# Kernel optimization log

Hardware: AMD Instinct MI355X
Metric: run time of the kernel (lower is better)

Reference implementation:

```python
import jax, jax.numpy as jnp
import numpy as np

B, S, D = 8, 1024, 1024
H = 16
D_HEAD = D // H
RANK = 256
NC = 64
NE = 64
KC = 16  # top_k_compress
KE = 8   # top_k_expand


def setup_inputs() -> dict:
    key = jax.random.key(0)
    ks = jax.random.split(key, 9)
    rn = lambda k, sh, s=1.0: jax.random.normal(k, sh, jnp.float32) * s
    return {
        "x": rn(ks[0], (B, S, D)),
        "importance": jax.random.uniform(ks[1], (B, S), jnp.float32),
        "W_compress": rn(ks[2], (NC, D), 1.0 / np.sqrt(D)),
        "W_Q": rn(ks[3], (NE, D), 1.0 / np.sqrt(D)),
        "W_K": rn(ks[4], (NE, D), 1.0 / np.sqrt(D)),
        "W_V": rn(ks[5], (NE, D), 1.0 / np.sqrt(D)),
        "compress_neurons": rn(ks[6], (NC, D, RANK), 1.0 / np.sqrt(D)),
        "expand_pool": rn(ks[7], (NE, RANK, D), 1.0 / np.sqrt(RANK)),
        "W_O": rn(ks[8], (D, D), 1.0 / np.sqrt(D)),
    }


def _route(x, importance, W, k):
    """Per-token softmax router, importance-aggregated, top-k renormalized."""
    pref = jax.nn.softmax(jnp.einsum('bsd,nd->bsn', x, W), axis=-1)  # [B,S,n]
    w = jnp.einsum('bs,bsn->bn', importance, pref)                   # [B,n]
    w = w / (w.sum(-1, keepdims=True) + 1e-8)
    tw, ti = jax.lax.top_k(w, k)                                     # [B,k]
    tw = tw / (tw.sum(-1, keepdims=True) + 1e-8)
    return tw, ti


def reference(x, importance, W_compress, W_Q, W_K, W_V, compress_neurons, expand_pool, W_O):
    # --- GlobalRouters.get_attention_weights ---
    cw, ci = _route(x, importance, W_compress, KC)
    qw, qi = _route(x, importance, W_Q, KE)
    kw, ki = _route(x, importance, W_K, KE)
    vw, vi = _route(x, importance, W_V, KE)

    # --- NeuronCircuit.forward ---
    # gather + mix compress neurons: [B,KC,D,R] -> [B,D,R]
    shared_c = jnp.einsum('bk,bkdr->bdr', cw, compress_neurons[ci])
    h = jnp.einsum('bsd,bdr->bsr', x, shared_c)  # [B,S,R]

    eQ = jnp.einsum('bk,bkrd->brd', qw, expand_pool[qi])
    eK = jnp.einsum('bk,bkrd->brd', kw, expand_pool[ki])
    eV = jnp.einsum('bk,bkrd->brd', vw, expand_pool[vi])

    def heads(t):  # [B,S,D] -> [B,H,S,d_head]
        return t.reshape(B, S, H, D_HEAD).transpose(0, 2, 1, 3)

    Q = heads(jnp.einsum('bsr,brd->bsd', h, eQ))
    K = heads(jnp.einsum('bsr,brd->bsd', h, eK))
    V = heads(jnp.einsum('bsr,brd->bsd', h, eV))

    scale = 1.0 / np.sqrt(D_HEAD)
    scores = jnp.einsum('bhqd,bhkd->bhqk', Q, K) * scale
    causal = jnp.tril(jnp.ones((S, S), dtype=bool))
    scores = jnp.where(causal, scores, jnp.finfo(scores.dtype).min)
    attn = jax.nn.softmax(scores, axis=-1)
    out = jnp.einsum('bhqk,bhkd->bhqd', attn, V)
    out = out.transpose(0, 2, 1, 3).reshape(B, S, D)
    return jnp.einsum('bsd,ed->bse', out, W_O)  # expand_O (Linear, no bias)
```

## Files before the change

kernel.cpp:

```cpp
#include <hip/hip_runtime.h>

typedef __attribute__((ext_vector_type(8))) short short8;
typedef __attribute__((ext_vector_type(4))) short short4v;
typedef __attribute__((ext_vector_type(4))) float f32x4;
typedef unsigned short u16;
typedef unsigned int u32;

__device__ __forceinline__ float bf2f(u16 h) {
    return __uint_as_float(((u32)h) << 16);
}
__device__ __forceinline__ u16 f2bf(float f) {
    u32 u = __float_as_uint(f);
    u32 r = u + 0x7fffu + ((u >> 16) & 1u);
    return (u16)(r >> 16);
}
__device__ __forceinline__ u32 pack_bf(float a, float b) {
    return __builtin_amdgcn_perm(__float_as_uint(b), __float_as_uint(a), 0x07060302u);
}

__device__ __forceinline__ void async_copy16(const void* g, void* l) {
    __builtin_amdgcn_global_load_lds(
        (const __attribute__((address_space(1))) void*)g,
        (__attribute__((address_space(3))) void*)l, 16, 0, 0);
}

__global__ __launch_bounds__(256) void cvt_split(
    const float* __restrict__ in, u16* __restrict__ hi, u16* __restrict__ lo, int n4)
{
    int i = blockIdx.x * 256 + threadIdx.x;
    if (i >= n4) return;
    float4 v = ((const float4*)in)[i];
    short4v h, l;
    float vv[4] = {v.x, v.y, v.z, v.w};
#pragma unroll
    for (int j = 0; j < 4; j++) {
        u16 hb = f2bf(vv[j]);
        h[j] = (short)hb;
        l[j] = (short)f2bf(vv[j] - bf2f(hb));
    }
    ((short4v*)hi)[i] = h;
    ((short4v*)lo)[i] = l;
}

__global__ __launch_bounds__(256) void cvt_split_w4(
    const float* __restrict__ w0, const float* __restrict__ w1,
    const float* __restrict__ w2, const float* __restrict__ w3,
    u16* __restrict__ hi, u16* __restrict__ lo)
{
    const int r = blockIdx.x >> 6;
    const float* src = (r == 0) ? w0 : (r == 1) ? w1 : (r == 2) ? w2 : w3;
    int i = (blockIdx.x & 63) * 256 + threadIdx.x;
    float4 v = ((const float4*)src)[i];
    short4v h, l;
    float vv[4] = {v.x, v.y, v.z, v.w};
#pragma unroll
    for (int j = 0; j < 4; j++) {
        u16 hb = f2bf(vv[j]);
        h[j] = (short)hb;
        l[j] = (short)f2bf(vv[j] - bf2f(hb));
    }
    ((short4v*)(hi + (long)r * 65536))[i] = h;
    ((short4v*)(lo + (long)r * 65536))[i] = l;
}

__global__ __launch_bounds__(256) void cvt_bf(
    const float* __restrict__ in, u16* __restrict__ out, int n4)
{
    int i = blockIdx.x * 256 + threadIdx.x;
    if (i >= n4) return;
    float4 v = ((const float4*)in)[i];
    short4v h;
    h[0] = (short)f2bf(v.x); h[1] = (short)f2bf(v.y);
    h[2] = (short)f2bf(v.z); h[3] = (short)f2bf(v.w);
    ((short4v*)out)[i] = h;
}

template <typename CT>
__global__ __launch_bounds__(256) void gemm_bt(
    const u16* __restrict__ A, long lda, long bsA,
    const u16* __restrict__ Bm, long ldb, long bsB,
    CT* __restrict__ C, long ldc, long bsC, int K, float cscale)
{
    __shared__ __align__(16) u16 lsA[128 * 64];
    __shared__ __align__(16) u16 lsB[128 * 64];
    const int tid = threadIdx.x;
    const int wave = tid >> 6, lane = tid & 63;
    const int quad = lane >> 4, l15 = lane & 15;
    const int wm = wave >> 1, wn = wave & 1;
    const long m0 = (long)blockIdx.x * 128, n0 = (long)blockIdx.y * 128;
    A  += (long)blockIdx.z * bsA;
    Bm += (long)blockIdx.z * bsB;
    C  += (long)blockIdx.z * bsC;
    const int srow = lane >> 2, scol = (lane & 3) * 8;

    f32x4 acc[4][4];
#pragma unroll
    for (int i = 0; i < 4; i++)
#pragma unroll
        for (int j = 0; j < 4; j++) acc[i][j] = (f32x4){0.f, 0.f, 0.f, 0.f};

    const u16* ga0 = A + (m0 + (wave * 2 + 0) * 16 + srow) * lda + scol;
    const u16* ga1 = A + (m0 + (wave * 2 + 1) * 16 + srow) * lda + scol;
    const u16* gb0 = Bm + (n0 + (wave * 2 + 0) * 16 + srow) * ldb + scol;
    const u16* gb1 = Bm + (n0 + (wave * 2 + 1) * 16 + srow) * ldb + scol;
    u16* laA = &lsA[(wave * 2 + 0) * 1024];
    u16* laB = &lsA[(wave * 2 + 1) * 1024];
    u16* lbA = &lsB[(wave * 2 + 0) * 1024];
    u16* lbB = &lsB[(wave * 2 + 1) * 1024];

    for (int kk = 0; kk < K; kk += 64) {
        async_copy16(ga0 + kk,      laA);
        async_copy16(ga0 + kk + 32, laA + 512);
        async_copy16(ga1 + kk,      laB);
        async_copy16(ga1 + kk + 32, laB + 512);
        async_copy16(gb0 + kk,      lbA);
        async_copy16(gb0 + kk + 32, lbA + 512);
        async_copy16(gb1 + kk,      lbB);
        async_copy16(gb1 + kk + 32, lbB + 512);
        __syncthreads();
#pragma unroll
        for (int kb = 0; kb < 2; kb++) {
            short8 af[4], bf[4];
#pragma unroll
            for (int mt = 0; mt < 4; mt++)
                af[mt] = *(const short8*)&lsA[(wm * 4 + mt) * 1024 + kb * 512 + l15 * 32 + quad * 8];
#pragma unroll
            for (int nt = 0; nt < 4; nt++)
                bf[nt] = *(const short8*)&lsB[(wn * 4 + nt) * 1024 + kb * 512 + l15 * 32 + quad * 8];
#pragma unroll
            for (int mt = 0; mt < 4; mt++)
#pragma unroll
                for (int nt = 0; nt < 4; nt++)
                    acc[mt][nt] = __builtin_amdgcn_mfma_f32_16x16x32_bf16(
                        af[mt], bf[nt], acc[mt][nt], 0, 0, 0);
        }
        __syncthreads();
    }
#pragma unroll
    for (int mt = 0; mt < 4; mt++) {
        const long rowb = m0 + wm * 64 + mt * 16 + quad * 4;
#pragma unroll
        for (int nt = 0; nt < 4; nt++) {
            const long col = n0 + wn * 64 + nt * 16 + l15;
#pragma unroll
            for (int r = 0; r < 4; r++) {
                const float v = acc[mt][nt][r] * cscale;
                if constexpr (sizeof(CT) == 2)
                    C[(rowb + r) * ldc + col] = f2bf(v);
                else
                    C[(rowb + r) * ldc + col] = v;
            }
        }
    }
}

__global__ __launch_bounds__(256) void gemm_qkv(
    const u16* __restrict__ hbuf, const u16* __restrict__ eQT,
    const u16* __restrict__ eKT, const u16* __restrict__ eVT,
    u16* __restrict__ Qb, u16* __restrict__ Kb, u16* __restrict__ VTb)
{
    __shared__ __align__(16) u16 lsA[128 * 64];
    __shared__ __align__(16) u16 lsB[128 * 64];
    const int z = blockIdx.z;
    const int sel = z >> 3, bbz = z & 7;
    const long ab = (long)bbz * 262144;
    const u16* A  = ((sel == 2) ? eVT : hbuf) + ab;
    const u16* Bm = ((sel == 0) ? eQT : (sel == 1) ? eKT : hbuf) + ab;
    u16* C = ((sel == 0) ? Qb : (sel == 1) ? Kb : VTb) + (long)bbz * 1048576;
    const float cscale = (sel == 0) ? 0.180336880111f : 1.0f;

    const int tid = threadIdx.x;
    const int wave = tid >> 6, lane = tid & 63;
    const int quad = lane >> 4, l15 = lane & 15;
    const int wm = wave >> 1, wn = wave & 1;
    const long m0 = (long)blockIdx.x * 128, n0 = (long)blockIdx.y * 128;
    const int srow = lane >> 2, scol = (lane & 3) * 8;

    f32x4 acc[4][4];
#pragma unroll
    for (int i = 0; i < 4; i++)
#pragma unroll
        for (int j = 0; j < 4; j++) acc[i][j] = (f32x4){0.f, 0.f, 0.f, 0.f};

    const u16* ga0 = A + (m0 + (wave * 2 + 0) * 16 + srow) * 256 + scol;
    const u16* ga1 = A + (m0 + (wave * 2 + 1) * 16 + srow) * 256 + scol;
    const u16* gb0 = Bm + (n0 + (wave * 2 + 0) * 16 + srow) * 256 + scol;
    const u16* gb1 = Bm + (n0 + (wave * 2 + 1) * 16 + srow) * 256 + scol;
    u16* laA = &lsA[(wave * 2 + 0) * 1024];
    u16* laB = &lsA[(wave * 2 + 1) * 1024];
    u16* lbA = &lsB[(wave * 2 + 0) * 1024];
    u16* lbB = &lsB[(wave * 2 + 1) * 1024];

    for (int kk = 0; kk < 256; kk += 64) {
        async_copy16(ga0 + kk,      laA);
        async_copy16(ga0 + kk + 32, laA + 512);
        async_copy16(ga1 + kk,      laB);
        async_copy16(ga1 + kk + 32, laB + 512);
        async_copy16(gb0 + kk,      lbA);
        async_copy16(gb0 + kk + 32, lbA + 512);
        async_copy16(gb1 + kk,      lbB);
        async_copy16(gb1 + kk + 32, lbB + 512);
        __syncthreads();
#pragma unroll
        for (int kb = 0; kb < 2; kb++) {
            short8 af[4], bf[4];
#pragma unroll
            for (int mt = 0; mt < 4; mt++)
                af[mt] = *(const short8*)&lsA[(wm * 4 + mt) * 1024 + kb * 512 + l15 * 32 + quad * 8];
#pragma unroll
            for (int nt = 0; nt < 4; nt++)
                bf[nt] = *(const short8*)&lsB[(wn * 4 + nt) * 1024 + kb * 512 + l15 * 32 + quad * 8];
#pragma unroll
            for (int mt = 0; mt < 4; mt++)
#pragma unroll
                for (int nt = 0; nt < 4; nt++)
                    acc[mt][nt] = __builtin_amdgcn_mfma_f32_16x16x32_bf16(
                        af[mt], bf[nt], acc[mt][nt], 0, 0, 0);
        }
        __syncthreads();
    }
#pragma unroll
    for (int mt = 0; mt < 4; mt++) {
        const long rowb = m0 + wm * 64 + mt * 16 + quad * 4;
#pragma unroll
        for (int nt = 0; nt < 4; nt++) {
            const long col = n0 + wn * 64 + nt * 16 + l15;
#pragma unroll
            for (int r = 0; r < 4; r++)
                C[(rowb + r) * 1024 + col] = f2bf(acc[mt][nt][r] * cscale);
        }
    }
}

__global__ __launch_bounds__(256) void gemm_router(
    const u16* __restrict__ Ah, const u16* __restrict__ Al,
    const u16* __restrict__ Bh, const u16* __restrict__ Bl,
    float* __restrict__ C0, float* __restrict__ C1, float* __restrict__ C2)
{
    __shared__ __align__(16) u16 lsA[128 * 64];
    __shared__ __align__(16) u16 lsB[128 * 64];
    const int seg = blockIdx.z;
    const u16* A = (seg == 1) ? Al : Ah;
    const u16* B = (seg == 2) ? Bl : Bh;
    float* C = (seg == 0) ? C0 : (seg == 1) ? C1 : C2;
    const int tid = threadIdx.x;
    const int wave = tid >> 6, lane = tid & 63;
    const int quad = lane >> 4, l15 = lane & 15;
    const int wm = wave >> 1, wn = wave & 1;
    const long m0 = (long)blockIdx.x * 128, n0 = (long)blockIdx.y * 128;
    const int srow = lane >> 2, scol = (lane & 3) * 8;
    const u16* ga = A + (m0 + (wave * 2) * 16 + srow) * 1024 + scol;
    const u16* gb = B + (n0 + (wave * 2) * 16 + srow) * 1024 + scol;
    u16* laA = &lsA[(wave * 2 + 0) * 1024];
    u16* laB = &lsA[(wave * 2 + 1) * 1024];
    u16* lbA = &lsB[(wave * 2 + 0) * 1024];
    u16* lbB = &lsB[(wave * 2 + 1) * 1024];

    f32x4 acc[4][4];
#pragma unroll
    for (int i = 0; i < 4; i++)
#pragma unroll
        for (int j = 0; j < 4; j++) acc[i][j] = (f32x4){0.f, 0.f, 0.f, 0.f};

    for (int kk = 0; kk < 1024; kk += 64) {
        async_copy16(ga + kk,              laA);
        async_copy16(ga + kk + 32,         laA + 512);
        async_copy16(ga + 16384 + kk,      laB);
        async_copy16(ga + 16384 + kk + 32, laB + 512);
        async_copy16(gb + kk,              lbA);
        async_copy16(gb + kk + 32,         lbA + 512);
        async_copy16(gb + 16384 + kk,      lbB);
        async_copy16(gb + 16384 + kk + 32, lbB + 512);
        __syncthreads();
#pragma unroll
        for (int kb = 0; kb < 2; kb++) {
            short8 af[4], bf[4];
#pragma unroll
            for (int mt = 0; mt < 4; mt++)
                af[mt] = *(const short8*)&lsA[(wm * 4 + mt) * 1024 + kb * 512 + l15 * 32 + quad * 8];
#pragma unroll
            for (int nt = 0; nt < 4; nt++)
                bf[nt] = *(const short8*)&lsB[(wn * 4 + nt) * 1024 + kb * 512 + l15 * 32 + quad * 8];
#pragma unroll
            for (int mt = 0; mt < 4; mt++)
#pragma unroll
                for (int nt = 0; nt < 4; nt++)
                    acc[mt][nt] = __builtin_amdgcn_mfma_f32_16x16x32_bf16(
                        af[mt], bf[nt], acc[mt][nt], 0, 0, 0);
        }
        __syncthreads();
    }
#pragma unroll
    for (int mt = 0; mt < 4; mt++) {
        const long rowb = m0 + wm * 64 + mt * 16 + quad * 4;
#pragma unroll
        for (int nt = 0; nt < 4; nt++) {
            const long col = n0 + wn * 64 + nt * 16 + l15;
#pragma unroll
            for (int r = 0; r < 4; r++)
                C[(rowb + r) * 256 + col] = acc[mt][nt][r];
        }
    }
}

__global__ __launch_bounds__(128) void router_agg(
    const float* __restrict__ l0, const float* __restrict__ l1,
    const float* __restrict__ l2, const float* __restrict__ imp,
    float* __restrict__ w_raw)
{
    __shared__ float pref[32][257];
    const int tid = threadIdx.x;
    const int tl = tid >> 2, r = tid & 3;
    const int s = blockIdx.x * 32 + tl;
    const int b = s >> 10;
    const long off = (long)s * 256 + r * 64;
    float v[64];
#pragma unroll
    for (int i = 0; i < 16; i++) {
        float4 f0 = ((const float4*)(l0 + off))[i];
        float4 f1 = ((const float4*)(l1 + off))[i];
        float4 f2 = ((const float4*)(l2 + off))[i];
        v[i * 4 + 0] = f0.x + f1.x + f2.x;
        v[i * 4 + 1] = f0.y + f1.y + f2.y;
        v[i * 4 + 2] = f0.z + f1.z + f2.z;
        v[i * 4 + 3] = f0.w + f1.w + f2.w;
    }
    float mx = v[0];
#pragma unroll
    for (int i = 1; i < 64; i++) mx = fmaxf(mx, v[i]);
    float sum = 0.f;
#pragma unroll
    for (int i = 0; i < 64; i++) { v[i] = __expf(v[i] - mx); sum += v[i]; }
    const float scale = imp[s] / sum;
#pragma unroll
    for (int i = 0; i < 64; i++) pref[tl][r * 64 + i] = v[i] * scale;
    __syncthreads();
#pragma unroll
    for (int half = 0; half < 2; half++) {
        const int idx = tid + half * 128;
        const int r2 = idx >> 6, n = idx & 63;
        float acc = 0.f;
#pragma unroll 8
        for (int t = 0; t < 32; t++) acc += pref[t][r2 * 64 + n];
        atomicAdd(&w_raw[(r2 * 8 + b) * 64 + n], acc);
    }
}

__global__ void topk_kernel(const float* __restrict__ w_raw,
                            float* __restrict__ topw, int* __restrict__ topi)
{
    const int r = blockIdx.x >> 3, b = blockIdx.x & 7;
    const int lane = threadIdx.x;
    const int k = (r == 0) ? 16 : 8;
    float w = w_raw[(r * 8 + b) * 64 + lane];
    float tot = w;
    for (int o2 = 32; o2 >= 1; o2 >>= 1) tot += __shfl_xor(tot, o2);
    w = w / (tot + 1e-8f);
    __shared__ float tw[16];
    __shared__ int ti[16];
    float cur = w;
    float ssum = 0.f;
    for (int j = 0; j < k; j++) {
        float m = cur; int mi = lane;
        for (int o2 = 32; o2 >= 1; o2 >>= 1) {
            float om = __shfl_xor(m, o2); int oi = __shfl_xor(mi, o2);
            if (om > m || (om == m && oi < mi)) { m = om; mi = oi; }
        }
        if (lane == 0) { tw[j] = m; ti[j] = mi; }
        ssum += m;
        if (lane == mi) cur = -1e30f;
    }
    __syncthreads();
    if (lane < 16) {
        topw[(r * 8 + b) * 16 + lane] = (lane < k) ? tw[lane] / (ssum + 1e-8f) : 0.f;
        topi[(r * 8 + b) * 16 + lane] = (lane < k) ? ti[lane] : 0;
    }
}

__global__ __launch_bounds__(256) void gather_mix(
    const float* __restrict__ pool, const float* __restrict__ topw,
    const int* __restrict__ topi, u16* __restrict__ out,
    int I, int J, int k)
{
    __shared__ float tile[64][65];
    const int b = blockIdx.z;
    const long IJ = (long)I * J;
    const int i0 = blockIdx.x * 64, j0 = blockIdx.y * 64;
    const float* tw = topw + b * 16;
    const int* ti = topi + b * 16;
    const int tid = threadIdx.x;
    const int il = tid >> 2, jg = tid & 3;
    float acc[16];
#pragma unroll
    for (int m = 0; m < 16; m++) acc[m] = 0.f;
    for (int kk = 0; kk < k; kk++) {
        const float wgt = tw[kk];
        const long n = ti[kk];
        const float* src = pool + n * IJ + (long)(i0 + il) * J + j0 + jg * 16;
        float4 a0 = ((const float4*)src)[0];
        float4 a1 = ((const float4*)src)[1];
        float4 a2 = ((const float4*)src)[2];
        float4 a3 = ((const float4*)src)[3];
        acc[0] += wgt * a0.x;  acc[1] += wgt * a0.y;
        acc[2] += wgt * a0.z;  acc[3] += wgt * a0.w;
        acc[4] += wgt * a1.x;  acc[5] += wgt * a1.y;
        acc[6] += wgt * a1.z;  acc[7] += wgt * a1.w;
        acc[8] += wgt * a2.x;  acc[9] += wgt * a2.y;
        acc[10] += wgt * a2.z; acc[11] += wgt * a2.w;
        acc[12] += wgt * a3.x; acc[13] += wgt * a3.y;
        acc[14] += wgt * a3.z; acc[15] += wgt * a3.w;
    }
#pragma unroll
    for (int m = 0; m < 16; m++) tile[il][jg * 16 + m] = acc[m];
    __syncthreads();
    const int jl = tid >> 2, ig = tid & 3;
    short8 o0, o1;
#pragma unroll
    for (int m = 0; m < 8; m++) {
        o0[m] = (short)f2bf(tile[ig * 16 + m][jl]);
        o1[m] = (short)f2bf(tile[ig * 16 + 8 + m][jl]);
    }
    u16* dst = out + (long)b * IJ + (long)(j0 + jl) * I + i0 + ig * 16;
    *(short8*)dst = o0;
    *(short8*)(dst + 8) = o1;
}

__global__ __launch_bounds__(256) void gather_mix3(
    const float* __restrict__ pool, const float* __restrict__ topw,
    const int* __restrict__ topi, u16* __restrict__ eQT,
    u16* __restrict__ eKT, u16* __restrict__ eVT)
{
    __shared__ float tile[64][65];
    const int z = blockIdx.z;
    const int r = z >> 3, b = z & 7;
    u16* out = (r == 0) ? eQT : (r == 1) ? eKT : eVT;
    const long IJ = 262144;
    const int i0 = blockIdx.x * 64, j0 = blockIdx.y * 64;
    const float* tw = topw + (1 + r) * 128 + b * 16;
    const int* ti = topi + (1 + r) * 128 + b * 16;
    const int tid = threadIdx.x;
    const int il = tid >> 2, jg = tid & 3;
    float acc[16];
#pragma unroll
    for (int m = 0; m < 16; m++) acc[m] = 0.f;
    for (int kk = 0; kk < 8; kk++) {
        const float wgt = tw[kk];
        const long n = ti[kk];
        const float* src = pool + n * IJ + (long)(i0 + il) * 1024 + j0 + jg * 16;
        float4 a0 = ((const float4*)src)[0];
        float4 a1 = ((const float4*)src)[1];
        float4 a2 = ((const float4*)src)[2];
        float4 a3 = ((const float4*)src)[3];
        acc[0] += wgt * a0.x;  acc[1] += wgt * a0.y;
        acc[2] += wgt * a0.z;  acc[3] += wgt * a0.w;
        acc[4] += wgt * a1.x;  acc[5] += wgt * a1.y;
        acc[6] += wgt * a1.z;  acc[7] += wgt * a1.w;
        acc[8] += wgt * a2.x;  acc[9] += wgt * a2.y;
        acc[10] += wgt * a2.z; acc[11] += wgt * a2.w;
        acc[12] += wgt * a3.x; acc[13] += wgt * a3.y;
        acc[14] += wgt * a3.z; acc[15] += wgt * a3.w;
    }
#pragma unroll
    for (int m = 0; m < 16; m++) tile[il][jg * 16 + m] = acc[m];
    __syncthreads();
    const int jl = tid >> 2, ig = tid & 3;
    short8 o0, o1;
#pragma unroll
    for (int m = 0; m < 8; m++) {
        o0[m] = (short)f2bf(tile[ig * 16 + m][jl]);
        o1[m] = (short)f2bf(tile[ig * 16 + 8 + m][jl]);
    }
    u16* dst = out + (long)b * IJ + (long)(j0 + jl) * 256 + i0 + ig * 16;
    *(short8*)dst = o0;
    *(short8*)(dst + 8) = o1;
}

__global__ __launch_bounds__(256, 2) void flash_attn(
    const u16* __restrict__ Qg, const u16* __restrict__ Kg,
    const u16* __restrict__ Vt, u16* __restrict__ Og)
{
    __shared__ __align__(16) u16 plds[4][32 * 72];
    const int tid = threadIdx.x;
    const int wv = tid >> 6, lane = tid & 63;
    const int quad = lane >> 4, l15 = lane & 15;
    const int p = blockIdx.x;
    const int bidx = (p & 7) * 64 + (p >> 3);
    const int gw = bidx * 4 + wv;
    const int pr = gw & 15;
    const int bh = gw >> 4;
    const int hh = bh & 15, bb = bh >> 4;
    const long SD = 1024L * 1024L;
    const u16* Qb = Qg + (long)bb * SD + hh * 64;
    const u16* Kb = Kg + (long)bb * SD + hh * 64;
    const u16* Vb = Vt + (long)bb * SD + (long)hh * 64 * 1024;
    u16* myp = plds[wv];

    for (int half = 0; half < 2; half++) {
        const int qt = half ? (31 - pr) : pr;
        const int q0 = qt * 32;

        short8 qf[2][2];
#pragma unroll
        for (int mt = 0; mt < 2; mt++)
#pragma unroll
            for (int kb = 0; kb < 2; kb++)
                qf[mt][kb] = *(const short8*)(Qb + (long)(q0 + mt * 16 + l15) * 1024 + kb * 32 + quad * 8);

        f32x4 o[2][4];
        float mrow[2] = {-3e38f, -3e38f}, lrow[2] = {0.f, 0.f};
#pragma unroll
        for (int mt = 0; mt < 2; mt++)
#pragma unroll
            for (int nt = 0; nt < 4; nt++) o[mt][nt] = (f32x4){0.f, 0.f, 0.f, 0.f};

        const int ntile = (q0 + 95) >> 6;
        short8 kf[4][2], kn[4][2];
#pragma unroll
        for (int kt = 0; kt < 4; kt++)
#pragma unroll
            for (int kb = 0; kb < 2; kb++)
                kf[kt][kb] = *(const short8*)(Kb + (long)(kt * 16 + l15) * 1024 + kb * 32 + quad * 8);

        for (int it = 0; it < ntile; it++) {
            const int k2 = it * 64;
            const bool last = (it == ntile - 1);
            f32x4 st[4][2];
            __builtin_amdgcn_s_setprio(1);
#pragma unroll
            for (int kt = 0; kt < 4; kt++)
#pragma unroll
                for (int q_ = 0; q_ < 2; q_++) {
                    f32x4 z = (f32x4){0.f, 0.f, 0.f, 0.f};
                    z = __builtin_amdgcn_mfma_f32_16x16x32_bf16(kf[kt][0], qf[q_][0], z, 0, 0, 0);
                    z = __builtin_amdgcn_mfma_f32_16x16x32_bf16(kf[kt][1], qf[q_][1], z, 0, 0, 0);
                    st[kt][q_] = z;
                }
            __builtin_amdgcn_s_setprio(0);
            short8 vf[4][2];
#pragma unroll
            for (int nt = 0; nt < 4; nt++)
#pragma unroll
                for (int kh = 0; kh < 2; kh++)
                    vf[nt][kh] = *(const short8*)(Vb + (long)(nt * 16 + l15) * 1024 + k2 + kh * 32 + quad * 8);
            if (it + 1 < ntile) {
#pragma unroll
                for (int kt = 0; kt < 4; kt++)
#pragma unroll
                    for (int kb = 0; kb < 2; kb++)
                        kn[kt][kb] = *(const short8*)(Kb + (long)(k2 + 64 + kt * 16 + l15) * 1024 + kb * 32 + quad * 8);
            }
            float am[2];
#pragma unroll
            for (int q_ = 0; q_ < 2; q_++) {
                if (last) {
#pragma unroll
                    for (int kt = 0; kt < 4; kt++)
#pragma unroll
                        for (int r = 0; r < 4; r++)
                            if (k2 + kt * 16 + quad * 4 + r > q0 + q_ * 16 + l15)
                                st[kt][q_][r] = -3e38f;
                }
                float t0 = fmaxf(fmaxf(st[0][q_][0], st[0][q_][1]), fmaxf(st[0][q_][2], st[0][q_][3]));
                float t1 = fmaxf(fmaxf(st[1][q_][0], st[1][q_][1]), fmaxf(st[1][q_][2], st[1][q_][3]));
                float t2 = fmaxf(fmaxf(st[2][q_][0], st[2][q_][1]), fmaxf(st[2][q_][2], st[2][q_][3]));
                float t3 = fmaxf(fmaxf(st[3][q_][0], st[3][q_][1]), fmaxf(st[3][q_][2], st[3][q_][3]));
                float cm = fmaxf(fmaxf(t0, t1), fmaxf(t2, t3));
                cm = fmaxf(cm, __shfl_xor(cm, 16));
                cm = fmaxf(cm, __shfl_xor(cm, 32));
                const float mn = fmaxf(mrow[q_], cm);
                am[q_] = exp2f(mrow[q_] - mn);
                mrow[q_] = mn;
                const float moff = 0.00281502f - mn;
                float s4[4];
#pragma unroll
                for (int kt = 0; kt < 4; kt++) {
                    float p0 = exp2f(st[kt][q_][0] + moff);
                    float p1 = exp2f(st[kt][q_][1] + moff);
                    float p2 = exp2f(st[kt][q_][2] + moff);
                    float p3 = exp2f(st[kt][q_][3] + moff);
                    s4[kt] = (p0 + p1) + (p2 + p3);
                    u32 w0 = pack_bf(p0, p1);
                    u32 w1 = pack_bf(p2, p3);
                    *(uint2*)&myp[(q_ * 16 + l15) * 72 + kt * 16 + quad * 4] = make_uint2(w0, w1);
                }
                float rs = (s4[0] + s4[1]) + (s4[2] + s4[3]);
                rs += __shfl_xor(rs, 16);
                rs += __shfl_xor(rs, 32);
                lrow[q_] = lrow[q_] * am[q_] + rs;
            }
            float av[2][4];
#pragma unroll
            for (int mt = 0; mt < 2; mt++)
#pragma unroll
                for (int r = 0; r < 4; r++)
                    av[mt][r] = __shfl(am[mt], quad * 4 + r);
            asm volatile("s_waitcnt lgkmcnt(0)" ::: "memory");
            short8 pf0[2], pf1[2];
#pragma unroll
            for (int kh = 0; kh < 2; kh++) {
                pf0[kh] = *(const short8*)&myp[(l15) * 72 + kh * 32 + quad * 8];
                pf1[kh] = *(const short8*)&myp[(16 + l15) * 72 + kh * 32 + quad * 8];
            }
#pragma unroll
            for (int mt = 0; mt < 2; mt++)
#pragma unroll
                for (int nt = 0; nt < 4; nt++)
#pragma unroll
                    for (int r = 0; r < 4; r++) o[mt][nt][r] *= av[mt][r];
            __builtin_amdgcn_s_setprio(1);
#pragma unroll
            for (int nt = 0; nt < 4; nt++)
#pragma unroll
                for (int kh = 0; kh < 2; kh++) {
                    o[0][nt] = __builtin_amdgcn_mfma_f32_16x16x32_bf16(pf0[kh], vf[nt][kh], o[0][nt], 0, 0, 0);
                    o[1][nt] = __builtin_amdgcn_mfma_f32_16x16x32_bf16(pf1[kh], vf[nt][kh], o[1][nt], 0, 0, 0);
                }
            __builtin_amdgcn_s_setprio(0);
            if (it + 1 < ntile) {
#pragma unroll
                for (int kt = 0; kt < 4; kt++)
#pragma unroll
                    for (int kb = 0; kb < 2; kb++) kf[kt][kb] = kn[kt][kb];
            }
        }
#pragma unroll
        for (int mt = 0; mt < 2; mt++)
#pragma unroll
            for (int r = 0; r < 4; r++) {
                const float li = 1.0f / __shfl(lrow[mt], quad * 4 + r);
                const long row = q0 + mt * 16 + quad * 4 + r;
#pragma unroll
                for (int nt = 0; nt < 4; nt++)
                    Og[(long)bb * SD + row * 1024 + hh * 64 + nt * 16 + l15] =
                        f2bf(o[mt][nt][r] * li);
            }
    }
}

extern "C" void kernel_launch(void* const* d_in, const int* in_sizes, int n_in,
                              void* d_out, int out_size, void* d_ws, size_t ws_size,
                              hipStream_t stream)
{
    const float* x   = (const float*)d_in[0];
    const float* imp = (const float*)d_in[1];
    const float* cn  = (const float*)d_in[6];
    const float* ep  = (const float*)d_in[7];
    const float* Wo  = (const float*)d_in[8];
    float* outp = (float*)d_out;
    char* ws = (char*)d_ws;

    u16* xh = (u16*)d_out;
    u16* xl = xh + 8388608;

    u16*   Wh     = (u16*)(ws + 0);
    u16*   Wl     = (u16*)(ws + 524288);
    u16*   Wobf   = (u16*)(ws + 1048576);
    float* w_raw  = (float*)(ws + 3145728);
    float* topw   = (float*)(ws + 3153920);
    int*   topi   = (int*)(ws + 3155968);
    float* logit0 = (float*)(ws + 4194304);
    float* logit1 = (float*)(ws + 33554432);
    float* logit2 = (float*)(ws + 41943040);
    u16*   scT    = (u16*)(ws + 12582912);
    u16*   eQT    = (u16*)(ws + 16777216);
    u16*   Kb     = (u16*)(ws + 4194304);
    u16*   hbuf   = (u16*)(ws + 20971520);
    u16*   eKT    = (u16*)(ws + 25165824);
    u16*   eVT    = (u16*)(ws + 29360128);
    u16*   Qb     = (u16*)(ws + 33554432);
    u16*   VTb    = (u16*)(ws + 50331648);
    u16*   aout   = (u16*)(ws + 67108864);

    cvt_split<<<dim3(8192), 256, 0, stream>>>(x, xh, xl, 2097152);
    cvt_split_w4<<<dim3(256), 256, 0, stream>>>(
        (const float*)d_in[2], (const float*)d_in[3],
        (const float*)d_in[4], (const float*)d_in[5], Wh, Wl);
    cvt_bf<<<dim3(1024), 256, 0, stream>>>(Wo, Wobf, 262144);
    hipMemsetAsync(w_raw, 0, 4 * 8 * 64 * 4, stream);

    gemm_router<<<dim3(64, 2, 3), 256, 0, stream>>>(
        xh, xl, Wh, Wl, logit0, logit1, logit2);
    router_agg<<<dim3(256), 128, 0, stream>>>(logit0, logit1, logit2, imp, w_raw);
    topk_kernel<<<dim3(32), 64, 0, stream>>>(w_raw, topw, topi);
    gather_mix<<<dim3(16, 4, 8), 256, 0, stream>>>(cn, topw + 0 * 128, topi + 0 * 128, scT, 1024, 256, 16);
    gather_mix3<<<dim3(4, 16, 24), 256, 0, stream>>>(ep, topw, topi, eQT, eKT, eVT);
    gemm_bt<u16><<<dim3(8, 2, 8), 256, 0, stream>>>(
        xh, 1024, 1048576, scT, 1024, 262144, hbuf, 256, 262144, 1024, 1.0f);
    gemm_qkv<<<dim3(8, 8, 24), 256, 0, stream>>>(hbuf, eQT, eKT, eVT, Qb, Kb, VTb);
    flash_attn<<<dim3(512), 256, 0, stream>>>(Qb, Kb, VTb, aout);
    gemm_bt<float><<<dim3(64, 8, 1), 256, 0, stream>>>(
        aout, 1024, 0, Wobf, 1024, 0, outp, 1024, 0, 1024, 1.0f);
}
```

Baseline: 404.2 us.

## Deepen GEMM K-tiles to 128 and skip flash-attention rescaling when max grows little

The generic bt GEMM is templated on the K-tile depth and the router GEMM is hardcoded to 128 instead of 64. This halves the number of barrier-separated load/compute iterations but doubles LDS use per block, which can cut occupancy. Separately, flash attention now keeps the old running max unless some row's max grows by more than 8 (in log2 units) across the wave. When no row passes that threshold, the per-row exp2 and the rescale of the output accumulator are skipped. Within that threshold the unnormalised exponentials can grow by up to 2^8 before normalisation, which still fits in fp32 and bf16 range.

Result: no change. 398.5 us (median of 2 runs) (-1.4%).

```diff
diff --git a/kernel.cpp b/kernel.cpp
--- a/kernel.cpp
+++ b/kernel.cpp
@@ -75,14 +75,16 @@
     ((short4v*)out)[i] = h;
 }
 
-template <typename CT>
+template <typename CT, int BK>
 __global__ __launch_bounds__(256) void gemm_bt(
     const u16* __restrict__ A, long lda, long bsA,
     const u16* __restrict__ Bm, long ldb, long bsB,
     CT* __restrict__ C, long ldc, long bsC, int K, float cscale)
 {
-    __shared__ __align__(16) u16 lsA[128 * 64];
-    __shared__ __align__(16) u16 lsB[128 * 64];
+    constexpr int NC = BK / 32;
+    constexpr int RB = 16 * BK;
+    __shared__ __align__(16) u16 lsA[128 * BK];
+    __shared__ __align__(16) u16 lsB[128 * BK];
     const int tid = threadIdx.x;
     const int wave = tid >> 6, lane = tid & 63;
     const int quad = lane >> 4, l15 = lane & 15;
@@ -103,30 +105,29 @@
     const u16* ga1 = A + (m0 + (wave * 2 + 1) * 16 + srow) * lda + scol;
     const u16* gb0 = Bm + (n0 + (wave * 2 + 0) * 16 + srow) * ldb + scol;
     const u16* gb1 = Bm + (n0 + (wave * 2 + 1) * 16 + srow) * ldb + scol;
-    u16* laA = &lsA[(wave * 2 + 0) * 1024];
-    u16* laB = &lsA[(wave * 2 + 1) * 1024];
-    u16* lbA = &lsB[(wave * 2 + 0) * 1024];
-    u16* lbB = &lsB[(wave * 2 + 1) * 1024];
-
-    for (int kk = 0; kk < K; kk += 64) {
-        async_copy16(ga0 + kk,      laA);
-        async_copy16(ga0 + kk + 32, laA + 512);
-        async_copy16(ga1 + kk,      laB);
-        async_copy16(ga1 + kk + 32, laB + 512);
-        async_copy16(gb0 + kk,      lbA);
-        async_copy16(gb0 + kk + 32, lbA + 512);
-        async_copy16(gb1 + kk,      lbB);
-        async_copy16(gb1 + kk + 32, lbB + 512);
+    u16* laA = &lsA[(wave * 2 + 0) * RB];
+    u16* laB = &lsA[(wave * 2 + 1) * RB];
+    u16* lbA = &lsB[(wave * 2 + 0) * RB];
+    u16* lbB = &lsB[(wave * 2 + 1) * RB];
+
+    for (int kk = 0; kk < K; kk += BK) {
+#pragma unroll
+        for (int c = 0; c < NC; c++) {
+            async_copy16(ga0 + kk + c * 32, laA + c * 512);
+            async_copy16(ga1 + kk + c * 32, laB + c * 512);
+            async_copy16(gb0 + kk + c * 32, lbA + c * 512);
+            async_copy16(gb1 + kk + c * 32, lbB + c * 512);
+        }
         __syncthreads();
 #pragma unroll
-        for (int kb = 0; kb < 2; kb++) {
+        for (int kb = 0; kb < NC; kb++) {
             short8 af[4], bf[4];
 #pragma unroll
             for (int mt = 0; mt < 4; mt++)
-                af[mt] = *(const short8*)&lsA[(wm * 4 + mt) * 1024 + kb * 512 + l15 * 32 + quad * 8];
+                af[mt] = *(const short8*)&lsA[(wm * 4 + mt) * RB + kb * 512 + l15 * 32 + quad * 8];
 #pragma unroll
             for (int nt = 0; nt < 4; nt++)
-                bf[nt] = *(const short8*)&lsB[(wn * 4 + nt) * 1024 + kb * 512 + l15 * 32 + quad * 8];
+                bf[nt] = *(const short8*)&lsB[(wn * 4 + nt) * RB + kb * 512 + l15 * 32 + quad * 8];
 #pragma unroll
             for (int mt = 0; mt < 4; mt++)
 #pragma unroll
@@ -237,8 +238,8 @@
     const u16* __restrict__ Bh, const u16* __restrict__ Bl,
     float* __restrict__ C0, float* __restrict__ C1, float* __restrict__ C2)
 {
-    __shared__ __align__(16) u16 lsA[128 * 64];
-    __shared__ __align__(16) u16 lsB[128 * 64];
+    __shared__ __align__(16) u16 lsA[128 * 128];
+    __shared__ __align__(16) u16 lsB[128 * 128];
     const int seg = blockIdx.z;
     const u16* A = (seg == 1) ? Al : Ah;
     const u16* B = (seg == 2) ? Bl : Bh;
@@ -251,10 +252,10 @@
     const int srow = lane >> 2, scol = (lane & 3) * 8;
     const u16* ga = A + (m0 + (wave * 2) * 16 + srow) * 1024 + scol;
     const u16* gb = B + (n0 + (wave * 2) * 16 + srow) * 1024 + scol;
-    u16* laA = &lsA[(wave * 2 + 0) * 1024];
-    u16* laB = &lsA[(wave * 2 + 1) * 1024];
-    u16* lbA = &lsB[(wave * 2 + 0) * 1024];
-    u16* lbB = &lsB[(wave * 2 + 1) * 1024];
+    u16* laA = &lsA[(wave * 2 + 0) * 2048];
+    u16* laB = &lsA[(wave * 2 + 1) * 2048];
+    u16* lbA = &lsB[(wave * 2 + 0) * 2048];
+    u16* lbB = &lsB[(wave * 2 + 1) * 2048];
 
     f32x4 acc[4][4];
 #pragma unroll
@@ -262,25 +263,24 @@
 #pragma unroll
         for (int j = 0; j < 4; j++) acc[i][j] = (f32x4){0.f, 0.f, 0.f, 0.f};
 
-    for (int kk = 0; kk < 1024; kk += 64) {
-        async_copy16(ga + kk,              laA);
-        async_copy16(ga + kk + 32,         laA + 512);
-        async_copy16(ga + 16384 + kk,      laB);
-        async_copy16(ga + 16384 + kk + 32, laB + 512);
-        async_copy16(gb + kk,              lbA);
-        async_copy16(gb + kk + 32,         lbA + 512);
-        async_copy16(gb + 16384 + kk,      lbB);
-        async_copy16(gb + 16384 + kk + 32, lbB + 512);
+    for (int kk = 0; kk < 1024; kk += 128) {
+#pragma unroll
+        for (int c = 0; c < 4; c++) {
+            async_copy16(ga + kk + c * 32,         laA + c * 512);
+            async_copy16(ga + 16384 + kk + c * 32, laB + c * 512);
+            async_copy16(gb + kk + c * 32,         lbA + c * 512);
+            async_copy16(gb + 16384 + kk + c * 32, lbB + c * 512);
+        }
         __syncthreads();
 #pragma unroll
-        for (int kb = 0; kb < 2; kb++) {
+        for (int kb = 0; kb < 4; kb++) {
             short8 af[4], bf[4];
 #pragma unroll
             for (int mt = 0; mt < 4; mt++)
-                af[mt] = *(const short8*)&lsA[(wm * 4 + mt) * 1024 + kb * 512 + l15 * 32 + quad * 8];
+                af[mt] = *(const short8*)&lsA[(wm * 4 + mt) * 2048 + kb * 512 + l15 * 32 + quad * 8];
 #pragma unroll
             for (int nt = 0; nt < 4; nt++)
-                bf[nt] = *(const short8*)&lsB[(wn * 4 + nt) * 1024 + kb * 512 + l15 * 32 + quad * 8];
+                bf[nt] = *(const short8*)&lsB[(wn * 4 + nt) * 2048 + kb * 512 + l15 * 32 + quad * 8];
 #pragma unroll
             for (int mt = 0; mt < 4; mt++)
 #pragma unroll
@@ -549,7 +549,7 @@
                     for (int kb = 0; kb < 2; kb++)
                         kn[kt][kb] = *(const short8*)(Kb + (long)(k2 + 64 + kt * 16 + l15) * 1024 + kb * 32 + quad * 8);
             }
-            float am[2];
+            float cm2[2];
 #pragma unroll
             for (int q_ = 0; q_ < 2; q_++) {
                 if (last) {
@@ -567,10 +567,22 @@
                 float cm = fmaxf(fmaxf(t0, t1), fmaxf(t2, t3));
                 cm = fmaxf(cm, __shfl_xor(cm, 16));
                 cm = fmaxf(cm, __shfl_xor(cm, 32));
-                const float mn = fmaxf(mrow[q_], cm);
-                am[q_] = exp2f(mrow[q_] - mn);
-                mrow[q_] = mn;
-                const float moff = 0.00281502f - mn;
+                cm2[q_] = cm;
+            }
+            const float grow = fmaxf(cm2[0] - mrow[0], cm2[1] - mrow[1]);
+            const bool resc = !__all(grow <= 8.0f);
+            float am[2] = {1.f, 1.f};
+            if (resc) {
+#pragma unroll
+                for (int q_ = 0; q_ < 2; q_++) {
+                    const float mn = fmaxf(mrow[q_], cm2[q_]);
+                    am[q_] = exp2f(mrow[q_] - mn);
+                    mrow[q_] = mn;
+                }
+            }
+#pragma unroll
+            for (int q_ = 0; q_ < 2; q_++) {
+                const float moff = 0.00281502f - mrow[q_];
                 float s4[4];
 #pragma unroll
                 for (int kt = 0; kt < 4; kt++) {
@@ -588,12 +600,20 @@
                 rs += __shfl_xor(rs, 32);
                 lrow[q_] = lrow[q_] * am[q_] + rs;
             }
-            float av[2][4];
-#pragma unroll
-            for (int mt = 0; mt < 2; mt++)
-#pragma unroll
-                for (int r = 0; r < 4; r++)
-                    av[mt][r] = __shfl(am[mt], quad * 4 + r);
+            if (resc) {
+                float av[2][4];
+#pragma unroll
+                for (int mt = 0; mt < 2; mt++)
+#pragma unroll
+                    for (int r = 0; r < 4; r++)
+                        av[mt][r] = __shfl(am[mt], quad * 4 + r);
+#pragma unroll
+                for (int mt = 0; mt < 2; mt++)
+#pragma unroll
+                    for (int nt = 0; nt < 4; nt++)
+#pragma unroll
+                        for (int r = 0; r < 4; r++) o[mt][nt][r] *= av[mt][r];
+            }
             asm volatile("s_waitcnt lgkmcnt(0)" ::: "memory");
             short8 pf0[2], pf1[2];
 #pragma unroll
@@ -601,12 +621,6 @@
                 pf0[kh] = *(const short8*)&myp[(l15) * 72 + kh * 32 + quad * 8];
                 pf1[kh] = *(const short8*)&myp[(16 + l15) * 72 + kh * 32 + quad * 8];
             }
-#pragma unroll
-            for (int mt = 0; mt < 2; mt++)
-#pragma unroll
-                for (int nt = 0; nt < 4; nt++)
-#pragma unroll
-                    for (int r = 0; r < 4; r++) o[mt][nt][r] *= av[mt][r];
             __builtin_amdgcn_s_setprio(1);
 #pragma unroll
             for (int nt = 0; nt < 4; nt++)
@@ -684,10 +698,10 @@
     topk_kernel<<<dim3(32), 64, 0, stream>>>(w_raw, topw, topi);
     gather_mix<<<dim3(16, 4, 8), 256, 0, stream>>>(cn, topw + 0 * 128, topi + 0 * 128, scT, 1024, 256, 16);
     gather_mix3<<<dim3(4, 16, 24), 256, 0, stream>>>(ep, topw, topi, eQT, eKT, eVT);
-    gemm_bt<u16><<<dim3(8, 2, 8), 256, 0, stream>>>(
+    gemm_bt<u16, 128><<<dim3(8, 2, 8), 256, 0, stream>>>(
         xh, 1024, 1048576, scT, 1024, 262144, hbuf, 256, 262144, 1024, 1.0f);
     gemm_qkv<<<dim3(8, 8, 24), 256, 0, stream>>>(hbuf, eQT, eKT, eVT, Qb, Kb, VTb);
     flash_attn<<<dim3(512), 256, 0, stream>>>(Qb, Kb, VTb, aout);
-    gemm_bt<float><<<dim3(64, 8, 1), 256, 0, stream>>>(
+    gemm_bt<float, 128><<<dim3(64, 8, 1), 256, 0, stream>>>(
         aout, 1024, 0, Wobf, 1024, 0, outp, 1024, 0, 1024, 1.0f);
 }
```
